# Optimization experiments

Measured on AMD Instinct MI355X. Metric: run time of the kernel, lower is better.

Reference implementation:

```python
import jax, jax.numpy as jnp
import numpy as np

BITS = 4
PACK = 32 // BITS  # 8 nibbles per int32
GROUP = 128
MASK = (1 << BITS) - 1


def _dequant(qweight, qzeros, scales):
    # qweight: [K//8, N] int32, nibbles packed along K (input) dim
    # qzeros : [G, N//8] int32, nibbles packed along N (output) dim
    # scales : [G, N] float
    shifts = jnp.arange(PACK, dtype=jnp.int32) * BITS  # [8]
    Kp, N = qweight.shape
    G = scales.shape[0]
    # unpack weights along input dim -> [K, N]
    w = (qweight[:, None, :] >> shifts[None, :, None]) & MASK  # [K//8, 8, N]
    w = w.reshape(Kp * PACK, N).astype(scales.dtype)
    # unpack zeros along output dim -> [G, N]
    z = (qzeros[:, :, None] >> shifts[None, None, :]) & MASK  # [G, N//8, 8]
    z = z.reshape(G, N).astype(scales.dtype) + 1.0  # GPTQ +1 zero offset
    # broadcast per-group zero/scale over GROUP consecutive input rows
    z_full = jnp.repeat(z, GROUP, axis=0)       # [K, N]
    s_full = jnp.repeat(scales, GROUP, axis=0)  # [K, N]
    return (w - z_full) * s_full  # [K, N]


def setup_inputs() -> dict:
    key = jax.random.key(0)
    k1, k2, k3, k4 = jax.random.split(key, 4)
    K, N, T = 4096, 11008, 8192
    x = jax.random.normal(k1, (T, K), dtype=jnp.float32)
    qweight = jax.random.randint(k2, (K // PACK, N), 0, 2147483647, dtype=jnp.int32)
    qzeros = jax.random.randint(k3, (K // GROUP, N // PACK), 0, 2147483647, dtype=jnp.int32)
    scales = jax.random.uniform(k4, (K // GROUP, N), dtype=jnp.float32) * 0.01
    return {"x": x, "qweight": qweight, "qzeros": qzeros, "scales": scales}


def reference(x, qweight, qzeros, scales):
    W = _dequant(qweight, qzeros, scales)  # [K, N]
    return x @ W  # [T, N]
```

## Files before the change

### kernel.cpp

```cpp
#include <hip/hip_runtime.h>
#include <hip/hip_bf16.h>
#include <cstdint>
#include <cstddef>


#define K_DIM 4096
#define N_DIM 11008
#define GROUP_SZ 128
#define KB (K_DIM * 2)
#define NTILES_K (K_DIM / 64)

typedef __bf16 bf16x8_t __attribute__((ext_vector_type(8)));
typedef float f32x4_t __attribute__((ext_vector_type(4)));

__device__ __forceinline__ void async_copy16(const void* g, void* l) {
    __builtin_amdgcn_global_load_lds((const __attribute__((address_space(1))) void*)g,
                                     (__attribute__((address_space(3))) void*)l,
                                     16, 0, 0);
}

__global__ __launch_bounds__(256) void convert_x_kernel(const float* __restrict__ x,
                                                        __bf16* __restrict__ xb,
                                                        long total) {
    long i = ((long)blockIdx.x * 256 + threadIdx.x) * 8;
    if (i >= total) return;
    const float4* p = (const float4*)(x + i);
    float4 u = p[0], v = p[1];
    bf16x8_t o;
    o[0] = (__bf16)u.x; o[1] = (__bf16)u.y; o[2] = (__bf16)u.z; o[3] = (__bf16)u.w;
    o[4] = (__bf16)v.x; o[5] = (__bf16)v.y; o[6] = (__bf16)v.z; o[7] = (__bf16)v.w;
    *(bf16x8_t*)(xb + i) = o;
}

__global__ __launch_bounds__(256) void dequant_kernel(const int* __restrict__ qw,
                                                      const int* __restrict__ qz,
                                                      const float* __restrict__ sc,
                                                      __bf16* __restrict__ Wt) {
    __shared__ __align__(16) __bf16 dqT[128 * 136];
    __shared__ float dqS[128];
    __shared__ float dqB[128];
    const int n0 = blockIdx.x * 128;
    const int g  = blockIdx.y;
    const int t  = threadIdx.x;

    if (t < 128) {
        int n = n0 + t;
        float s = sc[(size_t)g * N_DIM + n];
        int z = (qz[(size_t)g * (N_DIM / 8) + (n >> 3)] >> ((n & 7) * 4)) & 15;
        dqS[t] = s;
        dqB[t] = -(float)(z + 1) * s;
    }
    __syncthreads();

#pragma unroll
    for (int it = 0; it < 8; ++it) {
        int wi  = it * 256 + t;
        int row = wi >> 7;
        int col = wi & 127;
        int q = qw[(size_t)(g * 16 + row) * N_DIM + n0 + col];
        float s = dqS[col], b = dqB[col];
        bf16x8_t v;
#pragma unroll
        for (int j = 0; j < 8; ++j) {
            float w = (float)((q >> (4 * j)) & 15);
            v[j] = (__bf16)fmaf(w, s, b);
        }
        *(bf16x8_t*)(&dqT[col * 136 + row * 8]) = v;
    }
    __syncthreads();

    int n_loc = t & 127, half = t >> 7;
    const __bf16* src = &dqT[n_loc * 136 + half * 64];
    __bf16* dst = Wt + (size_t)(n0 + n_loc) * K_DIM + g * GROUP_SZ + half * 64;
#pragma unroll
    for (int i = 0; i < 8; ++i)
        *(bf16x8_t*)(dst + i * 8) = *(const bf16x8_t*)(src + i * 8);
}

__global__ __launch_bounds__(512, 2) void gemm256_kernel(const __bf16* __restrict__ A,
                                                         const __bf16* __restrict__ Bt,
                                                         float* __restrict__ C,
                                                         int mtiles, int ntiles) {
    __shared__ __align__(16) char ldsA[2][256 * 128];
    __shared__ __align__(16) char ldsB[2][256 * 128];
    const int tid = threadIdx.x;

    const int nwg = gridDim.x;
    const int bid = blockIdx.x;
    int vid = (nwg & 7) ? bid : ((bid & 7) * (nwg >> 3) + (bid >> 3));
    int mt, nt;
    if ((mtiles & 15) == 0) {
        const int bandsz = 16 * ntiles;
        const int band = vid / bandsz, rem = vid % bandsz;
        nt = rem >> 4;
        mt = (band << 4) + (rem & 15);
    } else {
        mt = vid % mtiles;
        nt = vid / mtiles;
    }

    const char* aPanel = (const char*)A + (size_t)mt * 256 * KB;
    const char* bPanel = (const char*)Bt + (size_t)nt * 256 * KB;

    int srcA[2], srcB[2], dstA[2], dstB[2];
#pragma unroll
    for (int q = 0; q < 2; ++q) {
        const int f = q * 512 + tid;
        const int r = f >> 3, c = f & 7;
        const int swz = (c * 16) ^ ((r & 7) << 4);
        const int Ra = r + (r & 64);
        const int Rb = r + (r & ~31);
        srcA[q] = Ra * KB + swz;  dstA[q] = Ra * 128 + c * 16;
        srcB[q] = Rb * KB + swz;  dstB[q] = Rb * 128 + c * 16;
    }

    const int lane = tid & 63;
    const int wid = tid >> 6;
    const int wm = wid >> 2, wn = wid & 3;
    const int lr = lane & 15, lq = lane >> 4;
    const int kOff0 = (lq * 16) ^ ((lr & 7) << 4);
    const int kOff1 = (64 + lq * 16) ^ ((lr & 7) << 4);
    const int aRowBase = wm * 128 + lr;
    const int bRowBase = wn * 64 + lr;

    bf16x8_t aF[4][2], bF[4][2];
    f32x4_t acc[8][4];
#pragma unroll
    for (int m = 0; m < 8; ++m)
#pragma unroll
        for (int n = 0; n < 4; ++n)
            acc[m][n] = (f32x4_t){0.f, 0.f, 0.f, 0.f};

#define GL_A(KT, BUFS, ROFF) do {                                                          \
    async_copy16(aPanel + (size_t)(KT) * 128 + (ROFF) * KB + srcA[0],                      \
                 &ldsA[BUFS][(ROFF) * 128] + dstA[0]);                                     \
    async_copy16(aPanel + (size_t)(KT) * 128 + (ROFF) * KB + srcA[1],                      \
                 &ldsA[BUFS][(ROFF) * 128] + dstA[1]);                                     \
} while (0)
#define GL_B(KT, BUFS, ROFF) do {                                                          \
    async_copy16(bPanel + (size_t)(KT) * 128 + (ROFF) * KB + srcB[0],                      \
                 &ldsB[BUFS][(ROFF) * 128] + dstB[0]);                                     \
    async_copy16(bPanel + (size_t)(KT) * 128 + (ROFF) * KB + srcB[1],                      \
                 &ldsB[BUFS][(ROFF) * 128] + dstB[1]);                                     \
} while (0)
#define READ_A(MQ, BUFC) do {                                                              \
    _Pragma("unroll") for (int i = 0; i < 4; ++i) {                                        \
        const char* _p = &ldsA[BUFC][(aRowBase + (MQ) * 64 + i * 16) * 128];               \
        aF[i][0] = *(const bf16x8_t*)(_p + kOff0);                                         \
        aF[i][1] = *(const bf16x8_t*)(_p + kOff1);                                         \
    }                                                                                      \
} while (0)
#define READ_B(NQ, BUFC) do {                                                              \
    _Pragma("unroll") for (int j = 0; j < 2; ++j) {                                        \
        const char* _p = &ldsB[BUFC][(bRowBase + ((NQ) * 2 + j) * 16) * 128];              \
        bF[(NQ) * 2 + j][0] = *(const bf16x8_t*)(_p + kOff0);                              \
        bF[(NQ) * 2 + j][1] = *(const bf16x8_t*)(_p + kOff1);                              \
    }                                                                                      \
} while (0)
#define MFMA_QUAD(MQ, NQ) do {                                                             \
    __builtin_amdgcn_s_setprio(1);                                                         \
    _Pragma("unroll") for (int kk = 0; kk < 2; ++kk)                                       \
    _Pragma("unroll") for (int i = 0; i < 4; ++i)                                          \
    _Pragma("unroll") for (int j = 0; j < 2; ++j)                                          \
        acc[(MQ) * 4 + i][(NQ) * 2 + j] = __builtin_amdgcn_mfma_f32_16x16x32_bf16(         \
            aF[i][kk], bF[(NQ) * 2 + j][kk], acc[(MQ) * 4 + i][(NQ) * 2 + j], 0, 0, 0);    \
    __builtin_amdgcn_s_setprio(0);                                                         \
} while (0)
#define BARRIER() asm volatile("s_barrier" ::: "memory")
#define VMCNT4()  asm volatile("s_waitcnt vmcnt(4)" ::: "memory")

#define KTILE(BUFC, KTS) do {                                                              \
                                                                      \
    READ_A(0, BUFC); READ_B(0, BUFC);                                                      \
    GL_A(KTS, (BUFC) ^ 1, 0);                                                              \
    VMCNT4(); BARRIER();                                                                   \
    MFMA_QUAD(0, 0);                                                                       \
                                                                      \
    READ_B(1, BUFC);                                                                       \
    GL_B(KTS, (BUFC) ^ 1, 0);                                                              \
    VMCNT4(); BARRIER();                                                                   \
    MFMA_QUAD(0, 1);                                                                       \
                                                                      \
    READ_A(1, BUFC);                                                                       \
    GL_B(KTS, (BUFC) ^ 1, 32);                                                             \
    BARRIER();                                                                             \
    MFMA_QUAD(1, 1);                                                                       \
                                       \
    GL_A(KTS, (BUFC) ^ 1, 64);                                                             \
    VMCNT4(); BARRIER();                                                                   \
    MFMA_QUAD(1, 0);                                                                       \
} while (0)

    GL_A(0, 0, 0); GL_B(0, 0, 0); GL_B(0, 0, 32); GL_A(0, 0, 64);
    VMCNT4(); BARRIER();

#pragma unroll 1
    for (int kt = 0; kt < NTILES_K; kt += 2) {
        const int ks0 = kt + 1;
        const int ks1 = (kt + 2 < NTILES_K) ? kt + 2 : kt + 1;
        KTILE(0, ks0);
        KTILE(1, ks1);
    }

    asm volatile("s_waitcnt vmcnt(0)" ::: "memory");

#pragma unroll
    for (int m = 0; m < 8; ++m) {
        const size_t gr = (size_t)mt * 256 + wm * 128 + m * 16 + lq * 4;
#pragma unroll
        for (int n = 0; n < 4; ++n) {
            const size_t gc = (size_t)nt * 256 + wn * 64 + n * 16 + lr;
            float* cp = C + gr * N_DIM + gc;
#pragma unroll
            for (int rg = 0; rg < 4; ++rg)
                cp[(size_t)rg * N_DIM] = acc[m][n][rg];
        }
    }
}

__global__ __launch_bounds__(256) void fallback_kernel(const float* __restrict__ x,
                                                       const int* __restrict__ qw,
                                                       const int* __restrict__ qz,
                                                       const float* __restrict__ sc,
                                                       float* __restrict__ out) {
    __shared__ float xrow[K_DIM];
    const int t = blockIdx.y;
    const int n = blockIdx.x * 256 + threadIdx.x;
    for (int i = threadIdx.x; i < K_DIM; i += 256)
        xrow[i] = x[(size_t)t * K_DIM + i];
    __syncthreads();
    if (n >= N_DIM) return;
    float acc = 0.f;
    for (int g = 0; g < K_DIM / GROUP_SZ; ++g) {
        float s = sc[(size_t)g * N_DIM + n];
        int z = (qz[(size_t)g * (N_DIM / 8) + (n >> 3)] >> ((n & 7) * 4)) & 15;
        float b = -(float)(z + 1) * s;
        for (int kp = g * 16; kp < g * 16 + 16; ++kp) {
            int q = qw[(size_t)kp * N_DIM + n];
#pragma unroll
            for (int j = 0; j < 8; ++j) {
                float w = (float)((q >> (4 * j)) & 15);
                acc = fmaf(xrow[kp * 8 + j], fmaf(w, s, b), acc);
            }
        }
    }
    out[(size_t)t * N_DIM + n] = acc;
}

extern "C" void kernel_launch(void* const* d_in, const int* in_sizes, int n_in,
                              void* d_out, int out_size, void* d_ws, size_t ws_size,
                              hipStream_t stream) {
    const float* x  = (const float*)d_in[0];
    const int*   qw = (const int*)d_in[1];
    const int*   qz = (const int*)d_in[2];
    const float* sc = (const float*)d_in[3];
    float* out = (float*)d_out;

    const long T = (long)in_sizes[0] / K_DIM;
    const size_t xb_bytes = (size_t)T * K_DIM * sizeof(__bf16);
    const size_t wt_bytes = (size_t)N_DIM * K_DIM * sizeof(__bf16);

    if (ws_size >= xb_bytes + wt_bytes && (T % 256) == 0) {
        __bf16* xb = (__bf16*)d_ws;
        __bf16* Wt = (__bf16*)((char*)d_ws + xb_bytes);
        long total = T * K_DIM;
        long nthr = total / 8;
        convert_x_kernel<<<dim3((unsigned)((nthr + 255) / 256)), dim3(256), 0, stream>>>(x, xb, total);
        dequant_kernel<<<dim3(N_DIM / 128, K_DIM / GROUP_SZ), dim3(256), 0, stream>>>(qw, qz, sc, Wt);
        const int mtiles = (int)(T / 256);
        const int ntiles = N_DIM / 256;
        gemm256_kernel<<<dim3((unsigned)(mtiles * ntiles)), dim3(512), 0, stream>>>(xb, Wt, out, mtiles, ntiles);
    } else {
        fallback_kernel<<<dim3(N_DIM / 256 + 1, (unsigned)T), dim3(256), 0, stream>>>(x, qw, qz, sc, out);
    }
}
```

Measured before the change: 749.7 us.

## Issue whole next K-tile prefetch up front with one barrier per tile

The async global-to-LDS copies for the next K tile are no longer spread across the four MFMA quadrants, each with its own partial vmcnt wait and barrier. All A and B copies for the next buffer are now issued at the start of each K tile, followed by a single vmcnt(0) wait and barrier at the end. The goal is to cut barrier and wait overhead and simplify the double-buffer schedule. The cost is losing the finer interleaving of loads with MFMA work, and the full drain of outstanding loads at each tile boundary may expose memory latency.

```diff
diff --git a/kernel.cpp b/kernel.cpp
--- a/kernel.cpp
+++ b/kernel.cpp
@@ -102,16 +102,13 @@
     const char* aPanel = (const char*)A + (size_t)mt * 256 * KB;
     const char* bPanel = (const char*)Bt + (size_t)nt * 256 * KB;
 
-    int srcA[2], srcB[2], dstA[2], dstB[2];
+    int srcO[2], dstO[2];
 #pragma unroll
     for (int q = 0; q < 2; ++q) {
         const int f = q * 512 + tid;
         const int r = f >> 3, c = f & 7;
         const int swz = (c * 16) ^ ((r & 7) << 4);
-        const int Ra = r + (r & 64);
-        const int Rb = r + (r & ~31);
-        srcA[q] = Ra * KB + swz;  dstA[q] = Ra * 128 + c * 16;
-        srcB[q] = Rb * KB + swz;  dstB[q] = Rb * 128 + c * 16;
+        srcO[q] = r * KB + swz;  dstO[q] = r * 128 + c * 16;
     }
 
     const int lane = tid & 63;
@@ -131,17 +128,17 @@
         for (int n = 0; n < 4; ++n)
             acc[m][n] = (f32x4_t){0.f, 0.f, 0.f, 0.f};
 
-#define GL_A(KT, BUFS, ROFF) do {                                                          \
-    async_copy16(aPanel + (size_t)(KT) * 128 + (ROFF) * KB + srcA[0],                      \
-                 &ldsA[BUFS][(ROFF) * 128] + dstA[0]);                                     \
-    async_copy16(aPanel + (size_t)(KT) * 128 + (ROFF) * KB + srcA[1],                      \
-                 &ldsA[BUFS][(ROFF) * 128] + dstA[1]);                                     \
-} while (0)
-#define GL_B(KT, BUFS, ROFF) do {                                                          \
-    async_copy16(bPanel + (size_t)(KT) * 128 + (ROFF) * KB + srcB[0],                      \
-                 &ldsB[BUFS][(ROFF) * 128] + dstB[0]);                                     \
-    async_copy16(bPanel + (size_t)(KT) * 128 + (ROFF) * KB + srcB[1],                      \
-                 &ldsB[BUFS][(ROFF) * 128] + dstB[1]);                                     \
+#define GL_TILE(KT, BUFS) do {                                                             \
+    _Pragma("unroll") for (int h = 0; h < 2; ++h) {                                        \
+        async_copy16(aPanel + (size_t)(KT) * 128 + h * 128 * KB + srcO[0],                 \
+                     &ldsA[BUFS][h * 128 * 128] + dstO[0]);                                \
+        async_copy16(aPanel + (size_t)(KT) * 128 + h * 128 * KB + srcO[1],                 \
+                     &ldsA[BUFS][h * 128 * 128] + dstO[1]);                                \
+        async_copy16(bPanel + (size_t)(KT) * 128 + h * 128 * KB + srcO[0],                 \
+                     &ldsB[BUFS][h * 128 * 128] + dstO[0]);                                \
+        async_copy16(bPanel + (size_t)(KT) * 128 + h * 128 * KB + srcO[1],                 \
+                     &ldsB[BUFS][h * 128 * 128] + dstO[1]);                                \
+    }                                                                                      \
 } while (0)
 #define READ_A(MQ, BUFC) do {                                                              \
     _Pragma("unroll") for (int i = 0; i < 4; ++i) {                                        \
@@ -167,32 +164,22 @@
     __builtin_amdgcn_s_setprio(0);                                                         \
 } while (0)
 #define BARRIER() asm volatile("s_barrier" ::: "memory")
-#define VMCNT4()  asm volatile("s_waitcnt vmcnt(4)" ::: "memory")
+#define VMCNT0()  asm volatile("s_waitcnt vmcnt(0)" ::: "memory")
 
 #define KTILE(BUFC, KTS) do {                                                              \
-                                                                      \
+    GL_TILE(KTS, (BUFC) ^ 1);                                                              \
     READ_A(0, BUFC); READ_B(0, BUFC);                                                      \
-    GL_A(KTS, (BUFC) ^ 1, 0);                                                              \
-    VMCNT4(); BARRIER();                                                                   \
     MFMA_QUAD(0, 0);                                                                       \
-                                                                      \
     READ_B(1, BUFC);                                                                       \
-    GL_B(KTS, (BUFC) ^ 1, 0);                                                              \
-    VMCNT4(); BARRIER();                                                                   \
     MFMA_QUAD(0, 1);                                                                       \
-                                                                      \
     READ_A(1, BUFC);                                                                       \
-    GL_B(KTS, (BUFC) ^ 1, 32);                                                             \
-    BARRIER();                                                                             \
     MFMA_QUAD(1, 1);                                                                       \
-                                       \
-    GL_A(KTS, (BUFC) ^ 1, 64);                                                             \
-    VMCNT4(); BARRIER();                                                                   \
     MFMA_QUAD(1, 0);                                                                       \
-} while (0)
-
-    GL_A(0, 0, 0); GL_B(0, 0, 0); GL_B(0, 0, 32); GL_A(0, 0, 64);
-    VMCNT4(); BARRIER();
+    VMCNT0(); BARRIER();                                                                   \
+} while (0)
+
+    GL_TILE(0, 0);
+    VMCNT0(); BARRIER();
 
 #pragma unroll 1
     for (int kt = 0; kt < NTILES_K; kt += 2) {
@@ -201,8 +188,6 @@
         KTILE(0, ks0);
         KTILE(1, ks1);
     }
-
-    asm volatile("s_waitcnt vmcnt(0)" ::: "memory");
 
 #pragma unroll
     for (int m = 0; m < 8; ++m) {
```

After: 810.0 us. 8.0% more time.
